# Performance work log

Hardware: AMD Instinct MI355X
Metric: run time of the kernel (lower is better)

The kernel has to match this reference:

```python
import math
import jax, jax.numpy as jnp
import numpy as np

D_MODEL = 2048
EXPAND = 2
D_INNER = EXPAND * D_MODEL          # 4096
HEADDIM = 64
NHEADS = D_INNER // HEADDIM          # 64
D_STATE = 128
CHUNK = 64
D_CONV = 4
NGROUPS = 1
X_PROJ_DIM = D_INNER + NHEADS + 2 * NGROUPS * D_STATE  # 4416
BATCH, SEQLEN = 2, 4096


def segsum(x):
    """Stable segment sum. x: (..., T) -> (..., T, T), lower-triangular, -inf above."""
    T = x.shape[-1]
    cs = jnp.cumsum(x, axis=-1)
    ss = cs[..., :, None] - cs[..., None, :]
    mask = jnp.tril(jnp.ones((T, T), dtype=bool))
    return jnp.where(mask, ss, -jnp.inf)


def ssd(X, A, B, C, block_len):
    """Chunked SSD scan (Mamba2). X:(b,l,gh,p) A:(b,l,gh) B,C:(b,l,g,n). fp32 math."""
    b, l = X.shape[0], X.shape[1]
    g = B.shape[2]
    h = X.shape[2] // g
    c = l // block_len
    X = X.astype(jnp.float32).reshape(b, c, block_len, g, h, HEADDIM)      # b c l g h p
    B = B.astype(jnp.float32).reshape(b, c, block_len, g, D_STATE)          # b c l g n
    C = C.astype(jnp.float32).reshape(b, c, block_len, g, D_STATE)
    A = A.astype(jnp.float32).reshape(b, c, block_len, g, h)
    A = jnp.transpose(A, (0, 3, 4, 1, 2))                                   # b g h c l
    A_cumsum = jnp.cumsum(A, axis=-1)
    L = jnp.exp(segsum(A))                                                  # b g h c l s
    # intra-chunk (diagonal) output
    Y_diag = jnp.einsum('bclgn,bcsgn,bghcls,bcsghp->bclghp', C, B, L, X)
    # per-chunk state contributions
    decay_states = jnp.exp(A_cumsum[..., -1:] - A_cumsum)                   # b g h c l
    states = jnp.einsum('bclgn,bghcl,bclghp->bcghpn', B, decay_states, X)
    init = jnp.zeros_like(states[:, :1])
    states = jnp.concatenate([init, states], axis=1)                         # b (c+1) g h p n
    chunk_A = jnp.pad(A_cumsum[..., -1], ((0, 0), (0, 0), (0, 0), (1, 0)))   # b g h (c+1)
    decay_chunk = jnp.exp(segsum(chunk_A))                                   # b g h (c+1) (c+1)
    new_states = jnp.einsum('bghzc,bcghpn->bzghpn', decay_chunk, states)
    states, final_state = new_states[:, :-1], new_states[:, -1]
    state_decay_out = jnp.exp(A_cumsum)                                      # b g h c l
    Y_off = jnp.einsum('bclgn,bcghpn,bghcl->bclghp', C, states, state_decay_out)
    Y = (Y_diag + Y_off).reshape(b, l, g * h, HEADDIM)
    final_state = final_state.reshape(b, g * h, HEADDIM, D_STATE)
    return Y, final_state


def setup_inputs() -> dict:
    key = jax.random.key(0)
    ks = jax.random.split(key, 8)
    s = 0.02
    u = jax.random.uniform(ks[6], (NHEADS,))
    dt0 = jnp.exp(u * (math.log(0.1) - math.log(0.001)) + math.log(0.001))
    inv_dt = dt0 + jnp.log(-jnp.expm1(-dt0))
    dt_std = NHEADS ** (-0.5)
    return {
        'x': jax.random.normal(ks[0], (BATCH, SEQLEN, D_MODEL), jnp.float32),
        'in_proj_w': jax.random.normal(ks[1], (2 * D_INNER, D_MODEL), jnp.float32) * s,
        'conv_w': jax.random.normal(ks[2], (D_INNER, D_CONV), jnp.float32) * s,
        'conv_b': jnp.zeros((D_INNER,), jnp.float32),
        'x_proj_w': jax.random.normal(ks[3], (X_PROJ_DIM, D_INNER), jnp.float32) * s,
        'dt_proj_w': jax.random.uniform(ks[4], (NHEADS, NHEADS), jnp.float32, -dt_std, dt_std),
        'dt_proj_b': inv_dt,
        'A_log': jnp.log(jnp.arange(1, NHEADS + 1, dtype=jnp.float32)),
        'D': jnp.ones((NHEADS,), jnp.float32),
        'out_proj_w': jax.random.normal(ks[5], (D_MODEL, D_INNER), jnp.float32) * s,
    }


def reference(x, in_proj_w, conv_w, conv_b, x_proj_w, dt_proj_w, dt_proj_b, A_log, D, out_proj_w):
    b, l, _ = x.shape
    xz = x @ in_proj_w.T                                   # (b,l,2*d_inner)
    x_branch, z_branch = jnp.split(xz, 2, axis=-1)
    # causal depthwise conv1d (pad left d_conv-1, truncate to seqlen)
    xt = jnp.transpose(x_branch, (0, 2, 1))                # (b,d_inner,l)
    kern = conv_w[:, None, :]                              # (d_inner,1,k)
    y = jax.lax.conv_general_dilated(
        xt, kern, window_strides=(1,), padding=[(D_CONV - 1, 0)],
        dimension_numbers=('NCH', 'OIH', 'NCH'), feature_group_count=D_INNER)
    x_branch = jnp.transpose(y + conv_b[None, :, None], (0, 2, 1))
    x_branch = jax.nn.silu(x_branch)
    proj = x_branch @ x_proj_w.T                           # (b,l,x_proj_dim)
    X = proj[..., :D_INNER].reshape(b, l, NHEADS, HEADDIM)
    dt = proj[..., D_INNER:D_INNER + NHEADS]
    Bm = proj[..., D_INNER + NHEADS:D_INNER + NHEADS + NGROUPS * D_STATE].reshape(b, l, NGROUPS, D_STATE)
    Cm = proj[..., D_INNER + NHEADS + NGROUPS * D_STATE:].reshape(b, l, NGROUPS, D_STATE)
    dt = jax.nn.softplus(dt @ dt_proj_w.T + dt_proj_b)      # (b,l,nheads)
    A = -jnp.exp(A_log)                                     # (nheads,)
    X_scaled = X * dt[..., None]
    A_scaled = A[None, None, :] * dt
    Y, _ = ssd(X_scaled, A_scaled, Bm, Cm, CHUNK)
    Y = Y.astype(x.dtype)
    Y = Y + X * D[None, None, :, None]
    Y = Y.reshape(b, l, D_INNER)
    Y = Y * jax.nn.silu(z_branch)
    return Y @ out_proj_w.T
```

## Files before the change

kernel.cpp:

```cpp
#include <hip/hip_runtime.h>

typedef __attribute__((ext_vector_type(8))) short short8;
typedef __attribute__((ext_vector_type(4))) short s16x4;
typedef __attribute__((ext_vector_type(4))) float f32x4;
typedef __attribute__((ext_vector_type(4))) unsigned int u32x4;

typedef __attribute__((address_space(3))) unsigned int lds_u32;
typedef __attribute__((address_space(1))) unsigned int glob_u32;

__device__ __forceinline__ float bf2f(unsigned short s) {
  unsigned int v = ((unsigned int)s) << 16; float f; __builtin_memcpy(&f, &v, 4); return f;
}
__device__ __forceinline__ unsigned short f2bf(float f) {
  unsigned int u; __builtin_memcpy(&u, &f, 4);
  u += 0x7fffu + ((u >> 16) & 1u);
  return (unsigned short)(u >> 16);
}
__device__ __forceinline__ unsigned int pack2bf(float lo, float hi) {
  return (unsigned int)f2bf(lo) | ((unsigned int)f2bf(hi) << 16);
}
__device__ __forceinline__ u32x4 pack8bf(f32x4 a, f32x4 b) {
  u32x4 r;
  r[0] = pack2bf(a[0], a[1]);
  r[1] = pack2bf(a[2], a[3]);
  r[2] = pack2bf(b[0], b[1]);
  r[3] = pack2bf(b[2], b[3]);
  return r;
}
__device__ __forceinline__ void ld8bf(const unsigned short* p, float* o) {
  short8 v = *(const short8*)p;
#pragma unroll
  for (int q = 0; q < 8; ++q) o[q] = bf2f((unsigned short)v[q]);
}
__device__ __forceinline__ void gl2lds16(const unsigned short* g, unsigned short* l) {
  __builtin_amdgcn_global_load_lds((const glob_u32*)g, (lds_u32*)l, 16, 0, 0);
}

#define LSEQ   4096
#define DMODEL 2048
#define DINNER 4096
#define NHEADS 64
#define PROJ_N 4416

__global__ void f2bf_kernel(const float* __restrict__ in, unsigned short* __restrict__ out, long n8) {
  long i = (long)blockIdx.x * blockDim.x + threadIdx.x;
  if (i >= n8) return;
  f32x4 a = *(const f32x4*)(in + i * 8);
  f32x4 b = *(const f32x4*)(in + i * 8 + 4);
  *(u32x4*)(out + i * 8) = pack8bf(a, b);
}

template <bool OUT_BF16>
__global__ __launch_bounds__(256) void gemm_bb(
    const unsigned short* __restrict__ A,
    const unsigned short* __restrict__ B,
    void* __restrict__ Cp, int K, int ldc, int nmax) {
  __shared__ __attribute__((aligned(16))) unsigned short Asm[128 * 32];
  __shared__ __attribute__((aligned(16))) unsigned short Bsm[128 * 32];
  const int tid = threadIdx.x;
  const int nbx = gridDim.x;
  int flat = blockIdx.y * nbx + blockIdx.x;
  const int nwg = nbx * gridDim.y;
  if ((nwg & 7) == 0) { const int cpx = nwg >> 3; flat = (flat & 7) * cpx + (flat >> 3); }
  const int m0 = (flat / nbx) * 128;
  const int n0 = (flat % nbx) * 128;

  const int wave = tid >> 6, lane = tid & 63;
  const int wm = (wave >> 1) * 64, wn = (wave & 1) * 64;
  const int quad = lane >> 4, l16 = lane & 15;
  const int rowL = tid >> 2;
  const int kk = (tid & 3) * 8;
  const long lK = K;

  int rb0 = n0 + rowL;      if (rb0 > nmax - 1) rb0 = nmax - 1;
  int rb1 = n0 + rowL + 64; if (rb1 > nmax - 1) rb1 = nmax - 1;
  const unsigned short* pa0 = A + (long)(m0 + rowL) * lK + kk;
  const unsigned short* pa1 = pa0 + 64 * lK;
  const unsigned short* pb0 = B + (long)rb0 * lK + kk;
  const unsigned short* pb1 = B + (long)rb1 * lK + kk;

  f32x4 zero = {0.f, 0.f, 0.f, 0.f};
  f32x4 acc[4][4];
#pragma unroll
  for (int i = 0; i < 4; ++i)
#pragma unroll
    for (int j = 0; j < 4; ++j) acc[i][j] = zero;

  for (int kt = 0; kt < K; kt += 32) {
    gl2lds16(pa0 + kt, Asm + tid * 8);
    gl2lds16(pa1 + kt, Asm + tid * 8 + 2048);
    gl2lds16(pb0 + kt, Bsm + tid * 8);
    gl2lds16(pb1 + kt, Bsm + tid * 8 + 2048);
    __syncthreads();
    short8 af[4], bfv[4];
#pragma unroll
    for (int i = 0; i < 4; ++i) {
      af[i]  = *(const short8*)(Asm + (wm + i * 16 + l16) * 32 + quad * 8);
      bfv[i] = *(const short8*)(Bsm + (wn + i * 16 + l16) * 32 + quad * 8);
    }
#pragma unroll
    for (int i = 0; i < 4; ++i)
#pragma unroll
      for (int j = 0; j < 4; ++j)
        acc[i][j] = __builtin_amdgcn_mfma_f32_16x16x32_bf16(af[i], bfv[j], acc[i][j], 0, 0, 0);
    __syncthreads();
  }

#pragma unroll
  for (int i = 0; i < 4; ++i) {
    const int mbase = m0 + wm + i * 16 + quad * 4;
#pragma unroll
    for (int j = 0; j < 4; ++j) {
      const int n = n0 + wn + j * 16 + l16;
      if (n < nmax) {
#pragma unroll
        for (int r = 0; r < 4; ++r) {
          const long o = (long)(mbase + r) * ldc + n;
          if (OUT_BF16) ((unsigned short*)Cp)[o] = f2bf(acc[i][j][r]);
          else          ((float*)Cp)[o] = acc[i][j][r];
        }
      }
    }
  }
}

template <bool A_F32, bool OUT_BF16>
__global__ __launch_bounds__(256) void gemm_nt(
    const void* __restrict__ Ap,
    const float* __restrict__ B,
    void* __restrict__ Cp, int K, int ldc, int nmax) {
  __shared__ __attribute__((aligned(16))) unsigned short Asm[128 * 32];
  __shared__ __attribute__((aligned(16))) unsigned short Bsm[128 * 32];
  const int tid = threadIdx.x;
  const int m0 = blockIdx.y * 128;
  const int n0 = blockIdx.x * 128;
  const int wave = tid >> 6, lane = tid & 63;
  const int wm = (wave >> 1) * 64, wn = (wave & 1) * 64;
  const int quad = lane >> 4, l16 = lane & 15;
  const int rowL = tid >> 2;
  const int kk = (tid & 3) * 8;
  const long lK = K;

  int rb0 = n0 + rowL;      if (rb0 > nmax - 1) rb0 = nmax - 1;
  int rb1 = n0 + rowL + 64; if (rb1 > nmax - 1) rb1 = nmax - 1;

  f32x4 zero = {0.f, 0.f, 0.f, 0.f};
  f32x4 acc[4][4];
#pragma unroll
  for (int i = 0; i < 4; ++i)
#pragma unroll
    for (int j = 0; j < 4; ++j) acc[i][j] = zero;

  for (int kt = 0; kt < K; kt += 32) {
    const float* pb0 = B + (long)rb0 * lK + kt + kk;
    const float* pb1 = B + (long)rb1 * lK + kt + kk;
    f32x4 b00 = *(const f32x4*)pb0;
    f32x4 b01 = *(const f32x4*)(pb0 + 4);
    f32x4 b10 = *(const f32x4*)pb1;
    f32x4 b11 = *(const f32x4*)(pb1 + 4);
    u32x4 bw0 = pack8bf(b00, b01);
    u32x4 bw1 = pack8bf(b10, b11);
    u32x4 aw0, aw1;
    if (A_F32) {
      const float* pa = (const float*)Ap + (long)(m0 + rowL) * lK + kt + kk;
      f32x4 a00 = *(const f32x4*)pa;
      f32x4 a01 = *(const f32x4*)(pa + 4);
      f32x4 a10 = *(const f32x4*)(pa + 64 * lK);
      f32x4 a11 = *(const f32x4*)(pa + 64 * lK + 4);
      aw0 = pack8bf(a00, a01);
      aw1 = pack8bf(a10, a11);
    } else {
      const unsigned short* pa = (const unsigned short*)Ap + (long)(m0 + rowL) * lK + kt + kk;
      aw0 = *(const u32x4*)pa;
      aw1 = *(const u32x4*)(pa + 64 * lK);
    }
    *(u32x4*)(Asm + tid * 8) = aw0;
    *(u32x4*)(Asm + tid * 8 + 2048) = aw1;
    *(u32x4*)(Bsm + tid * 8) = bw0;
    *(u32x4*)(Bsm + tid * 8 + 2048) = bw1;
    __syncthreads();
    short8 af[4], bfv[4];
#pragma unroll
    for (int i = 0; i < 4; ++i) {
      af[i]  = *(const short8*)(Asm + (wm + i * 16 + l16) * 32 + quad * 8);
      bfv[i] = *(const short8*)(Bsm + (wn + i * 16 + l16) * 32 + quad * 8);
    }
#pragma unroll
    for (int i = 0; i < 4; ++i)
#pragma unroll
      for (int j = 0; j < 4; ++j)
        acc[i][j] = __builtin_amdgcn_mfma_f32_16x16x32_bf16(af[i], bfv[j], acc[i][j], 0, 0, 0);
    __syncthreads();
  }

#pragma unroll
  for (int i = 0; i < 4; ++i) {
    const int mbase = m0 + wm + i * 16 + quad * 4;
#pragma unroll
    for (int j = 0; j < 4; ++j) {
      const int n = n0 + wn + j * 16 + l16;
      if (n < nmax) {
#pragma unroll
        for (int r = 0; r < 4; ++r) {
          const long o = (long)(mbase + r) * ldc + n;
          if (OUT_BF16) ((unsigned short*)Cp)[o] = f2bf(acc[i][j][r]);
          else          ((float*)Cp)[o] = acc[i][j][r];
        }
      }
    }
  }
}

__global__ void conv_silu_kernel(const unsigned short* __restrict__ xin,
                                 const float* __restrict__ cw,
                                 const float* __restrict__ cb,
                                 unsigned short* __restrict__ xout, long nv) {
  long idx = (long)blockIdx.x * blockDim.x + threadIdx.x;
  if (idx >= nv) return;
  int c8 = (int)(idx & 511);
  long row = idx >> 9;
  int l = (int)(row & (LSEQ - 1));
  int ch0 = c8 * 8;
  float acc[8];
#pragma unroll
  for (int q = 0; q < 8; ++q) acc[q] = cb[ch0 + q];
#pragma unroll
  for (int t = 0; t < 4; ++t) {
    int ll = l - 3 + t;
    if (ll >= 0) {
      float f[8];
      ld8bf(xin + (row - 3 + t) * 4096 + ch0, f);
#pragma unroll
      for (int q = 0; q < 8; ++q) acc[q] += f[q] * cw[(ch0 + q) * 4 + t];
    }
  }
  short8 o;
#pragma unroll
  for (int q = 0; q < 8; ++q) {
    float a = acc[q] / (1.f + expf(-acc[q]));
    o[q] = (short)f2bf(a);
  }
  *(short8*)(xout + row * 4096 + ch0) = o;
}

__global__ void dt_kernel(const unsigned short* __restrict__ proj,
                          const float* __restrict__ dtw,
                          const float* __restrict__ dtb,
                          float* __restrict__ dt, long n) {
  long idx = (long)blockIdx.x * blockDim.x + threadIdx.x;
  if (idx >= n) return;
  int h = (int)(idx & 63);
  long row = idx >> 6;
  const unsigned short* p = proj + row * PROJ_N + DINNER;
  float s = dtb[h];
#pragma unroll
  for (int k8 = 0; k8 < 8; ++k8) {
    float f[8];
    ld8bf(p + k8 * 8, f);
    const float* wv = dtw + h * 64 + k8 * 8;
#pragma unroll
    for (int q = 0; q < 8; ++q) s += f[q] * wv[q];
  }
  dt[idx] = (s > 20.f) ? s : log1pf(expf(s));
}


__global__ __launch_bounds__(256) void ssd_states_kernel(
    const unsigned short* __restrict__ proj,
    const float* __restrict__ dtbuf,
    const float* __restrict__ A_log,
    float* __restrict__ states,
    float* __restrict__ chdec) {
  __shared__ float Bs[64][132];
  __shared__ float Xw[64][68];
  __shared__ float csh[64];
  __shared__ float dth[64];
  const int tid = threadIdx.x;
  const int gc = blockIdx.x;
  const int h  = blockIdx.y;
  const long rowbase = (long)gc * 64;

  const float negA = -expf(A_log[h]);
  if (tid < 64) {
    float d = dtbuf[(rowbase + tid) * 64 + h];
    float v = negA * d;
#pragma unroll
    for (int off = 1; off < 64; off <<= 1) {
      float t = __shfl_up(v, off);
      if (tid >= off) v += t;
    }
    csh[tid] = v;
    dth[tid] = d;
  }
  __syncthreads();
  const float cs63 = csh[63];

  for (int idx = tid; idx < 64 * 16; idx += 256) {
    int r = idx >> 4, c8 = idx & 15;
    float f[8];
    ld8bf(proj + (rowbase + r) * PROJ_N + 4160 + c8 * 8, f);
#pragma unroll
    for (int q = 0; q < 8; ++q) Bs[r][c8 * 8 + q] = f[q];
  }
  for (int idx = tid; idx < 64 * 8; idx += 256) {
    int r = idx >> 3, c8 = idx & 7;
    float f[8];
    ld8bf(proj + (rowbase + r) * PROJ_N + h * 64 + c8 * 8, f);
    float w = dth[r] * expf(cs63 - csh[r]);
#pragma unroll
    for (int q = 0; q < 8; ++q) Xw[r][c8 * 8 + q] = w * f[q];
  }
  __syncthreads();

  const int p0 = (tid >> 4) * 4;
  const int n0 = (tid & 15) * 4;
  float a0[4][4] = {};
  float a1[4][4] = {};
  for (int j = 0; j < 64; ++j) {
    f32x4 xv = *(const f32x4*)&Xw[j][p0];
    f32x4 b0 = *(const f32x4*)&Bs[j][n0];
    f32x4 b1 = *(const f32x4*)&Bs[j][n0 + 64];
#pragma unroll
    for (int pp = 0; pp < 4; ++pp)
#pragma unroll
      for (int q = 0; q < 4; ++q) {
        a0[pp][q] += xv[pp] * b0[q];
        a1[pp][q] += xv[pp] * b1[q];
      }
  }
  float* sb = states + ((long)gc * 64 + h) * 8192;
#pragma unroll
  for (int q = 0; q < 4; ++q) {
    f32x4 t0, t1;
#pragma unroll
    for (int pp = 0; pp < 4; ++pp) { t0[pp] = a0[pp][q]; t1[pp] = a1[pp][q]; }
    *(f32x4*)(sb + (n0 + q) * 64 + p0) = t0;
    *(f32x4*)(sb + (n0 + 64 + q) * 64 + p0) = t1;
  }
  if (tid == 0) chdec[gc * 64 + h] = expf(cs63);
}

__global__ __launch_bounds__(256) void ssd_scan_kernel(
    float* __restrict__ states, const float* __restrict__ chdec) {
  const int by = blockIdx.y;
  const int b = by >> 6, h = by & 63;
  const int pn = blockIdx.x * 256 + threadIdx.x;
  float P = 0.f;
  long base = ((long)b * 64 * 64 + h) * 8192 + pn;
  for (int c = 0; c < 64; ++c) {
    long o = base + (long)c * (64 * 8192);
    float S = states[o];
    states[o] = P;
    P = chdec[(b * 64 + c) * 64 + h] * P + S;
  }
}

__global__ __launch_bounds__(512, 4) void ssd_ydo_gate_kernel(
    const unsigned short* __restrict__ proj,
    const float* __restrict__ dtbuf,
    const float* __restrict__ A_log,
    const float* __restrict__ Dv,
    const float* __restrict__ states,
    unsigned short* __restrict__ zio) {
  __shared__ __attribute__((aligned(16))) char smem[76800];
  float (*Cs)[68]          = (float(*)[68])(smem);
  float (*Scm)[68]         = (float(*)[68])(smem + 17408);
  unsigned short (*Xb)[72] = (unsigned short(*)[72])(smem + 34816);
  float* Pt                = (float*)(smem + 44032);
  float (*BsU)[68]         = (float(*)[68])(smem + 44032);

  const int tid = threadIdx.x;
  const int lane = tid & 63;
  const int gc = blockIdx.x;
  const int hbase = blockIdx.y * 16;
  const long rowbase = (long)gc * 64;

#pragma unroll
  for (int k = 0; k < 2; ++k) {
    int idx = tid + k * 512;
    int r = idx >> 4, c8 = idx & 15;
    const unsigned short* rp = proj + (rowbase + r) * PROJ_N;
    float fB[8], fC[8];
    ld8bf(rp + 4160 + c8 * 8, fB);
    ld8bf(rp + 4288 + c8 * 8, fC);
    f32x4 b0, b1, c0, c1;
#pragma unroll
    for (int q = 0; q < 4; ++q) { b0[q] = fB[q]; b1[q] = fB[q + 4]; c0[q] = fC[q]; c1[q] = fC[q + 4]; }
    *(f32x4*)&BsU[r][c8 * 8] = b0;
    *(f32x4*)&BsU[r][c8 * 8 + 4] = b1;
    *(f32x4*)&Cs[r][c8 * 8] = c0;
    *(f32x4*)&Cs[r][c8 * 8 + 4] = c1;
  }
  __syncthreads();

  const int iS = tid >> 3, t7 = tid & 7;
  float dm[8] = {};
  for (int n8 = 0; n8 < 16; ++n8) {
    f32x4 cv0 = *(const f32x4*)&Cs[iS][n8 * 8];
    f32x4 cv1 = *(const f32x4*)&Cs[iS][n8 * 8 + 4];
#pragma unroll
    for (int q = 0; q < 8; ++q) {
      int j = t7 + q * 8;
      f32x4 bv0 = *(const f32x4*)&BsU[j][n8 * 8];
      f32x4 bv1 = *(const f32x4*)&BsU[j][n8 * 8 + 4];
      dm[q] += cv0[0] * bv0[0] + cv0[1] * bv0[1] + cv0[2] * bv0[2] + cv0[3] * bv0[3]
             + cv1[0] * bv1[0] + cv1[1] * bv1[1] + cv1[2] * bv1[2] + cv1[3] * bv1[3];
    }
  }
  __syncthreads();

  const int i0 = (tid >> 4) * 2;
  const int p0 = (tid & 15) * 4;

  for (int hh = 0; hh < 16; ++hh) {
    const int h = hbase + hh;
    const float Dh = Dv[h];
    const float negA = -expf(A_log[h]);

    const float* sb2 = states + ((long)gc * 64 + h) * 8192;
    f32x4 s0 = *(const f32x4*)(sb2 + tid * 4);
    f32x4 s1 = *(const f32x4*)(sb2 + 2048 + tid * 4);
    f32x4 s2 = *(const f32x4*)(sb2 + 4096 + tid * 4);
    f32x4 s3 = *(const f32x4*)(sb2 + 6144 + tid * 4);
    short8 x8 = *(const short8*)(proj + (rowbase + iS) * PROJ_N + h * 64 + t7 * 8);
    float d = dtbuf[(rowbase + lane) * 64 + h];

    float v = negA * d;
    {
      float t;
      t = __shfl_up(v, 1);  if (lane >= 1)  v += t;
      t = __shfl_up(v, 2);  if (lane >= 2)  v += t;
      t = __shfl_up(v, 4);  if (lane >= 4)  v += t;
      t = __shfl_up(v, 8);  if (lane >= 8)  v += t;
      t = __shfl_up(v, 16); if (lane >= 16) v += t;
      t = __shfl_up(v, 32); if (lane >= 32) v += t;
    }

    *(f32x4*)&Pt[tid * 4]        = s0;
    *(f32x4*)&Pt[2048 + tid * 4] = s1;
    *(f32x4*)&Pt[4096 + tid * 4] = s2;
    *(f32x4*)&Pt[6144 + tid * 4] = s3;
    *(short8*)&Xb[iS][t7 * 8] = x8;
    {
      const float ci = __shfl(v, iS);
#pragma unroll
      for (int q = 0; q < 8; ++q) {
        int j = t7 + q * 8;
        float cj = __shfl(v, j);
        float dj = __shfl(d, j);
        Scm[iS][j] = (j <= iS) ? dm[q] * expf(ci - cj) * dj : 0.f;
      }
    }
    __syncthreads();

    const long r0w = rowbase + i0, r1w = r0w + 1;
    const long zo0 = r0w * 4096 + h * 64 + p0;
    const long zo1 = r1w * 4096 + h * 64 + p0;
    s16x4 zv0 = *(const s16x4*)&zio[zo0];
    s16x4 zv1 = *(const s16x4*)&zio[zo1];
    s16x4 xv0 = *(const s16x4*)(proj + r0w * PROJ_N + h * 64 + p0);
    s16x4 xv1 = *(const s16x4*)(proj + r1w * PROJ_N + h * 64 + p0);

    float ya0[4] = {}, ya1[4] = {};
#pragma unroll 4
    for (int j = 0; j < 64; ++j) {
      float sc0 = Scm[i0][j], sc1 = Scm[i0 + 1][j];
      s16x4 xj = *(const s16x4*)&Xb[j][p0];
#pragma unroll
      for (int k = 0; k < 4; ++k) {
        float xv = bf2f((unsigned short)xj[k]);
        ya0[k] += sc0 * xv;
        ya1[k] += sc1 * xv;
      }
    }
    float yb0[4] = {}, yb1[4] = {};
#pragma unroll 2
    for (int n8 = 0; n8 < 16; ++n8) {
      f32x4 ca0 = *(const f32x4*)&Cs[i0][n8 * 8];
      f32x4 ca1 = *(const f32x4*)&Cs[i0][n8 * 8 + 4];
      f32x4 cb0 = *(const f32x4*)&Cs[i0 + 1][n8 * 8];
      f32x4 cb1 = *(const f32x4*)&Cs[i0 + 1][n8 * 8 + 4];
#pragma unroll
      for (int q = 0; q < 8; ++q) {
        f32x4 pv = *(const f32x4*)&Pt[(n8 * 8 + q) * 64 + p0];
        float c0 = (q < 4) ? ca0[q] : ca1[q - 4];
        float c1 = (q < 4) ? cb0[q] : cb1[q - 4];
#pragma unroll
        for (int k = 0; k < 4; ++k) {
          yb0[k] += c0 * pv[k];
          yb1[k] += c1 * pv[k];
        }
      }
    }
    const float e0 = expf(__shfl(v, i0));
    const float e1 = expf(__shfl(v, i0 + 1));
    s16x4 o0, o1;
#pragma unroll
    for (int k = 0; k < 4; ++k) {
      float y = ya0[k] + e0 * yb0[k];
      float xraw = bf2f((unsigned short)xv0[k]);
      float zz = bf2f((unsigned short)zv0[k]);
      float sz = zz / (1.f + expf(-zz));
      o0[k] = (short)f2bf((y + xraw * Dh) * sz);
      y = ya1[k] + e1 * yb1[k];
      xraw = bf2f((unsigned short)xv1[k]);
      zz = bf2f((unsigned short)zv1[k]);
      sz = zz / (1.f + expf(-zz));
      o1[k] = (short)f2bf((y + xraw * Dh) * sz);
    }
    *(s16x4*)&zio[zo0] = o0;
    *(s16x4*)&zio[zo1] = o1;
    __syncthreads();
  }
}

__global__ __launch_bounds__(512) void ssd_gate_kernel(
    const unsigned short* __restrict__ proj,
    const float* __restrict__ dtbuf,
    const float* __restrict__ A_log,
    const float* __restrict__ Dv,
    unsigned short* __restrict__ zio) {
  __shared__ float st[64][128];
  __shared__ float Bs[64][128];
  __shared__ float Cs[64][128];
  __shared__ float Xs[64][64];
  __shared__ float Sc[64][64];
  __shared__ float cs[64];
  __shared__ float dtc[64];

  const int tid = threadIdx.x;
  const int bl = blockIdx.x >> 6;
  const int h = blockIdx.x & 63;
  const float negA = -expf(A_log[h]);
  const float Dh = Dv[h];

  for (int i = tid; i < 64 * 128; i += 512) (&st[0][0])[i] = 0.f;

  for (int c = 0; c < 64; ++c) {
    const long rowbase = (long)bl * LSEQ + c * 64;
    if (tid < 64) dtc[tid] = dtbuf[(rowbase + tid) * 64 + h];
    __syncthreads();
    if (tid == 0) {
      float run = 0.f;
      for (int j = 0; j < 64; ++j) { run += negA * dtc[j]; cs[j] = run; }
    }
    {
      const int j = tid >> 3;
      const int c8 = tid & 7;
      const unsigned short* rp = proj + (rowbase + j) * PROJ_N;
      const float dj = dtc[j];
#pragma unroll
      for (int q = 0; q < 8; ++q)
        Xs[j][c8 * 8 + q] = bf2f(rp[h * 64 + c8 * 8 + q]) * dj;
#pragma unroll
      for (int q = 0; q < 16; ++q) {
        Bs[j][c8 * 16 + q] = bf2f(rp[4160 + c8 * 16 + q]);
        Cs[j][c8 * 16 + q] = bf2f(rp[4288 + c8 * 16 + q]);
      }
    }
    __syncthreads();
    {
      const int i0 = (tid >> 4) * 2;
      const int j0 = (tid & 15) * 4;
      float a[2][4] = {};
      for (int n = 0; n < 128; ++n) {
        float c0 = Cs[i0][n], c1 = Cs[i0 + 1][n];
        float b0 = Bs[j0][n], b1 = Bs[j0 + 1][n], b2 = Bs[j0 + 2][n], b3 = Bs[j0 + 3][n];
        a[0][0] += c0 * b0; a[0][1] += c0 * b1; a[0][2] += c0 * b2; a[0][3] += c0 * b3;
        a[1][0] += c1 * b0; a[1][1] += c1 * b1; a[1][2] += c1 * b2; a[1][3] += c1 * b3;
      }
#pragma unroll
      for (int ii = 0; ii < 2; ++ii)
#pragma unroll
        for (int jj = 0; jj < 4; ++jj) {
          int i = i0 + ii, j = j0 + jj;
          Sc[i][j] = (j <= i) ? a[ii][jj] * expf(cs[i] - cs[j]) : 0.f;
        }
    }
    __syncthreads();
    {
      const int i0 = (tid >> 4) * 2;
      const int p0 = (tid & 15) * 4;
      float a1[2][4] = {};
      for (int j = 0; j < 64; ++j) {
        float s0 = Sc[i0][j], s1 = Sc[i0 + 1][j];
        float x0 = Xs[j][p0], x1 = Xs[j][p0 + 1], x2 = Xs[j][p0 + 2], x3 = Xs[j][p0 + 3];
        a1[0][0] += s0 * x0; a1[0][1] += s0 * x1; a1[0][2] += s0 * x2; a1[0][3] += s0 * x3;
        a1[1][0] += s1 * x0; a1[1][1] += s1 * x1; a1[1][2] += s1 * x2; a1[1][3] += s1 * x3;
      }
      float a2[2][4] = {};
      for (int n = 0; n < 128; ++n) {
        float c0 = Cs[i0][n], c1 = Cs[i0 + 1][n];
        float t0 = st[p0][n], t1 = st[p0 + 1][n], t2 = st[p0 + 2][n], t3 = st[p0 + 3][n];
        a2[0][0] += c0 * t0; a2[0][1] += c0 * t1; a2[0][2] += c0 * t2; a2[0][3] += c0 * t3;
        a2[1][0] += c1 * t0; a2[1][1] += c1 * t1; a2[1][2] += c1 * t2; a2[1][3] += c1 * t3;
      }
      float e0 = expf(cs[i0]), e1 = expf(cs[i0 + 1]);
#pragma unroll
      for (int ii = 0; ii < 2; ++ii) {
        const long r = rowbase + i0 + ii;
        const long zo = r * 4096 + h * 64 + p0;
        const unsigned short* xr = proj + r * PROJ_N + h * 64 + p0;
        float e = ii ? e1 : e0;
#pragma unroll
        for (int pp = 0; pp < 4; ++pp) {
          float y = a1[ii][pp] + e * a2[ii][pp];
          float xraw = bf2f(xr[pp]);
          float zz = bf2f(zio[zo + pp]);
          float sz = zz / (1.f + expf(-zz));
          zio[zo + pp] = f2bf((y + xraw * Dh) * sz);
        }
      }
    }
    __syncthreads();
    {
      const int j = tid >> 3;
      const int p0 = (tid & 7) * 8;
      float f = expf(cs[63] - cs[j]);
#pragma unroll
      for (int q = 0; q < 8; ++q) Xs[j][p0 + q] *= f;
    }
    __syncthreads();
    {
      const float dec = expf(cs[63]);
      const int p0 = (tid >> 5) * 4;
      const int n0 = (tid & 31) * 4;
      float a[4][4] = {};
      for (int j = 0; j < 64; ++j) {
        float x0 = Xs[j][p0], x1 = Xs[j][p0 + 1], x2 = Xs[j][p0 + 2], x3 = Xs[j][p0 + 3];
        float b0 = Bs[j][n0], b1 = Bs[j][n0 + 1], b2 = Bs[j][n0 + 2], b3 = Bs[j][n0 + 3];
        a[0][0] += x0 * b0; a[0][1] += x0 * b1; a[0][2] += x0 * b2; a[0][3] += x0 * b3;
        a[1][0] += x1 * b0; a[1][1] += x1 * b1; a[1][2] += x1 * b2; a[1][3] += x1 * b3;
        a[2][0] += x2 * b0; a[2][1] += x2 * b1; a[2][2] += x2 * b2; a[2][3] += x2 * b3;
        a[3][0] += x3 * b0; a[3][1] += x3 * b1; a[3][2] += x3 * b2; a[3][3] += x3 * b3;
      }
#pragma unroll
      for (int pp = 0; pp < 4; ++pp)
#pragma unroll
        for (int nn = 0; nn < 4; ++nn)
          st[p0 + pp][n0 + nn] = dec * st[p0 + pp][n0 + nn] + a[pp][nn];
    }
    __syncthreads();
  }
}

extern "C" void kernel_launch(void* const* d_in, const int* in_sizes, int n_in,
                              void* d_out, int out_size, void* d_ws, size_t ws_size,
                              hipStream_t stream) {
  (void)in_sizes; (void)n_in; (void)out_size;
  const float* x    = (const float*)d_in[0];
  const float* w1   = (const float*)d_in[1];
  const float* cw   = (const float*)d_in[2];
  const float* cb   = (const float*)d_in[3];
  const float* w2   = (const float*)d_in[4];
  const float* dtw  = (const float*)d_in[5];
  const float* dtb  = (const float*)d_in[6];
  const float* Alog = (const float*)d_in[7];
  const float* Dv   = (const float*)d_in[8];
  const float* w3   = (const float*)d_in[9];
  float* out = (float*)d_out;

  const size_t NEED8 = 410025984ull;
  const size_t NEED4 = 205012992ull;
  int CR; bool newpath;
  if      (ws_size >= NEED8)               { CR = 8192; newpath = true;  }
  else if (ws_size >= NEED4)               { CR = 4096; newpath = true;  }
  else if (ws_size >= (size_t)8192 * 17280){ CR = 8192; newpath = false; }
  else if (ws_size >= (size_t)4096 * 17280){ CR = 4096; newpath = false; }
  else return;

  char* w = (char*)d_ws;
  const size_t S1 = (size_t)CR * 4096 * 2;
  const size_t S2 = (size_t)CR * PROJ_N * 2;
  const int nb = CR / LSEQ;
  unsigned short* xc   = (unsigned short*)(w);
  unsigned short* xp   = (unsigned short*)(w + S1);
  unsigned short* proj = (unsigned short*)(w + S1);
  unsigned short* z    = (unsigned short*)(w);
  float* dtf           = (float*)(w + S1 + S2);
  float* chdec         = (float*)(w + S1 + S2 + (size_t)CR * 256);
  float* states        = (float*)(w + S1 + S2 + (size_t)CR * 256 + (size_t)nb * 16384);

  unsigned short* xbf  = (unsigned short*)states;
  unsigned short* w1bf = xbf + (size_t)CR * 2048;
  unsigned short* w2bf = w1bf + (size_t)8192 * 2048;
  unsigned short* w3bf = (unsigned short*)states;

  for (int r0 = 0; r0 < 8192; r0 += CR) {
    const float* xr = x + (size_t)r0 * DMODEL;
    dim3 g1(DINNER / 128, CR / 128);
    dim3 g2((PROJ_N + 127) / 128, CR / 128);
    dim3 g3(DMODEL / 128, CR / 128);
    if (newpath) {
      f2bf_kernel<<<((long)CR * 2048 / 8 + 255) / 256, 256, 0, stream>>>(xr, xbf, (long)CR * 2048 / 8);
      f2bf_kernel<<<((long)8192 * 2048 / 8 + 255) / 256, 256, 0, stream>>>(w1, w1bf, (long)8192 * 2048 / 8);
      f2bf_kernel<<<((long)4416 * 4096 / 8 + 255) / 256, 256, 0, stream>>>(w2, w2bf, (long)4416 * 4096 / 8);
      gemm_bb<true><<<g1, 256, 0, stream>>>(xbf, w1bf, xp, DMODEL, DINNER, DINNER);
      conv_silu_kernel<<<((long)CR * 512) / 256, 256, 0, stream>>>(xp, cw, cb, xc, (long)CR * 512);
      gemm_bb<true><<<g2, 256, 0, stream>>>(xc, w2bf, proj, DINNER, PROJ_N, PROJ_N);
      dt_kernel<<<((long)CR * NHEADS) / 256, 256, 0, stream>>>(proj, dtw, dtb, dtf, (long)CR * NHEADS);
      gemm_bb<true><<<g1, 256, 0, stream>>>(xbf, w1bf + (size_t)DINNER * DMODEL, z, DMODEL, DINNER, DINNER);
      ssd_states_kernel<<<dim3(nb * 64, 64), 256, 0, stream>>>(proj, dtf, Alog, states, chdec);
      ssd_scan_kernel<<<dim3(32, nb * 64), 256, 0, stream>>>(states, chdec);
      ssd_ydo_gate_kernel<<<dim3(nb * 64, 4), 512, 0, stream>>>(proj, dtf, Alog, Dv, states, z);
      f2bf_kernel<<<((long)2048 * 4096 / 8 + 255) / 256, 256, 0, stream>>>(w3, w3bf, (long)2048 * 4096 / 8);
      gemm_bb<false><<<g3, 256, 0, stream>>>(z, w3bf, out + (size_t)r0 * DMODEL, DINNER, DMODEL, DMODEL);
    } else {
      gemm_nt<true, true><<<g1, 256, 0, stream>>>(xr, w1, xp, DMODEL, DINNER, DINNER);
      conv_silu_kernel<<<((long)CR * 512) / 256, 256, 0, stream>>>(xp, cw, cb, xc, (long)CR * 512);
      gemm_nt<false, true><<<g2, 256, 0, stream>>>(xc, w2, proj, DINNER, PROJ_N, PROJ_N);
      dt_kernel<<<((long)CR * NHEADS) / 256, 256, 0, stream>>>(proj, dtw, dtb, dtf, (long)CR * NHEADS);
      gemm_nt<true, true><<<g1, 256, 0, stream>>>(xr, w1 + (size_t)DINNER * DMODEL, z, DMODEL, DINNER, DINNER);
      ssd_gate_kernel<<<(CR / LSEQ) * NHEADS, 512, 0, stream>>>(proj, dtf, Alog, Dv, z);
      gemm_nt<false, false><<<g3, 256, 0, stream>>>(z, w3, out + (size_t)r0 * DMODEL, DINNER, DMODEL, DMODEL);
    }
  }
}
```

Baseline: 2.156 ms.

## Replace bf16 GEMM with 256x256-tile double-buffered swizzled-LDS pipelined kernel

Replaces the 128x128, single-buffered, K=32 bf16 GEMM with a 256x256-tile, 512-thread kernel that uses K=64 steps and double-buffered 128KB LDS. Global-to-LDS loads are interleaved with MFMA sub-phases and tracked by explicit vmcnt waits and barriers. LDS addresses are XOR-swizzled to avoid bank conflicts, and s_setprio is raised around the MFMA phases. The aim is to overlap memory traffic with compute and increase data reuse. In exchange it adds register and LDS pressure, and the manual waitcnt and barrier sequencing is fragile.

Measured after the change: 1.921 ms. 10.9% less time.

```diff
diff --git a/kernel.cpp b/kernel.cpp
--- a/kernel.cpp
+++ b/kernel.cpp
@@ -50,78 +50,143 @@
   *(u32x4*)(out + i * 8) = pack8bf(a, b);
 }
 
-template <bool OUT_BF16>
-__global__ __launch_bounds__(256) void gemm_bb(
+#define CFENCE asm volatile("" ::: "memory")
+#define BARRIER do { CFENCE; __builtin_amdgcn_s_barrier(); CFENCE; } while (0)
+#define VMW(n) asm volatile("s_waitcnt vmcnt(" #n ")" ::: "memory")
+
+template <int MODE>
+__global__ __launch_bounds__(512, 2) void gemm256(
     const unsigned short* __restrict__ A,
     const unsigned short* __restrict__ B,
     void* __restrict__ Cp, int K, int ldc, int nmax) {
-  __shared__ __attribute__((aligned(16))) unsigned short Asm[128 * 32];
-  __shared__ __attribute__((aligned(16))) unsigned short Bsm[128 * 32];
+  __shared__ __attribute__((aligned(16))) char smem[131072];
   const int tid = threadIdx.x;
   const int nbx = gridDim.x;
   int flat = blockIdx.y * nbx + blockIdx.x;
   const int nwg = nbx * gridDim.y;
   if ((nwg & 7) == 0) { const int cpx = nwg >> 3; flat = (flat & 7) * cpx + (flat >> 3); }
-  const int m0 = (flat / nbx) * 128;
-  const int n0 = (flat % nbx) * 128;
+  const int m0 = (flat / nbx) * 256;
+  const int n0 = (flat % nbx) * 256;
 
   const int wave = tid >> 6, lane = tid & 63;
-  const int wm = (wave >> 1) * 64, wn = (wave & 1) * 64;
+  const int wm = wave >> 2;
+  const int wn = wave & 3;
   const int quad = lane >> 4, l16 = lane & 15;
-  const int rowL = tid >> 2;
-  const int kk = (tid & 3) * 8;
+
+  const int r0 = tid >> 3;
+  const int kboff = ((tid & 7) ^ (r0 & 7)) * 8;
   const long lK = K;
-
-  int rb0 = n0 + rowL;      if (rb0 > nmax - 1) rb0 = nmax - 1;
-  int rb1 = n0 + rowL + 64; if (rb1 > nmax - 1) rb1 = nmax - 1;
-  const unsigned short* pa0 = A + (long)(m0 + rowL) * lK + kk;
-  const unsigned short* pa1 = pa0 + 64 * lK;
-  const unsigned short* pb0 = B + (long)rb0 * lK + kk;
-  const unsigned short* pb1 = B + (long)rb1 * lK + kk;
-
-  f32x4 zero = {0.f, 0.f, 0.f, 0.f};
-  f32x4 acc[4][4];
-#pragma unroll
-  for (int i = 0; i < 4; ++i)
-#pragma unroll
-    for (int j = 0; j < 4; ++j) acc[i][j] = zero;
-
-  for (int kt = 0; kt < K; kt += 32) {
-    gl2lds16(pa0 + kt, Asm + tid * 8);
-    gl2lds16(pa1 + kt, Asm + tid * 8 + 2048);
-    gl2lds16(pb0 + kt, Bsm + tid * 8);
-    gl2lds16(pb1 + kt, Bsm + tid * 8 + 2048);
-    __syncthreads();
-    short8 af[4], bfv[4];
-#pragma unroll
-    for (int i = 0; i < 4; ++i) {
-      af[i]  = *(const short8*)(Asm + (wm + i * 16 + l16) * 32 + quad * 8);
-      bfv[i] = *(const short8*)(Bsm + (wn + i * 16 + l16) * 32 + quad * 8);
-    }
-#pragma unroll
-    for (int i = 0; i < 4; ++i)
-#pragma unroll
-      for (int j = 0; j < 4; ++j)
-        acc[i][j] = __builtin_amdgcn_mfma_f32_16x16x32_bf16(af[i], bfv[j], acc[i][j], 0, 0, 0);
-    __syncthreads();
-  }
-
-#pragma unroll
-  for (int i = 0; i < 4; ++i) {
-    const int mbase = m0 + wm + i * 16 + quad * 4;
+  const unsigned short* pa[4];
+  const unsigned short* pb[4];
+#pragma unroll
+  for (int h2 = 0; h2 < 4; ++h2) {
+    pa[h2] = A + (long)(m0 + h2 * 64 + r0) * lK + kboff;
+    int br = n0 + h2 * 64 + r0; if (br > nmax - 1) br = nmax - 1;
+    pb[h2] = B + (long)br * lK + kboff;
+  }
+  char* ldsp = (char*)smem;
+  const int ldst = tid * 16;
+
+#define STG_A(b, h, kt) do { \
+    gl2lds16(pa[(h)*2]     + (long)(kt) * 64, (unsigned short*)(ldsp + (b)*65536 + (h)*16384 + ldst)); \
+    gl2lds16(pa[(h)*2 + 1] + (long)(kt) * 64, (unsigned short*)(ldsp + (b)*65536 + (h)*16384 + 8192 + ldst)); \
+  } while (0)
+#define STG_B(b, h, kt) do { \
+    gl2lds16(pb[(h)*2]     + (long)(kt) * 64, (unsigned short*)(ldsp + (b)*65536 + 32768 + (h)*16384 + ldst)); \
+    gl2lds16(pb[(h)*2 + 1] + (long)(kt) * 64, (unsigned short*)(ldsp + (b)*65536 + 32768 + (h)*16384 + 8192 + ldst)); \
+  } while (0)
+
+  const int xm = (l16 & 7) << 4;
+  const int cb0 = (quad * 16) ^ xm;
+  const int cb1 = cb0 ^ 64;
+  const int aoff = (wm * 128 + l16) * 128;
+  const int boff = 32768 + (wn * 64 + l16) * 128;
+
+  f32x4 acc[8][4];
+  {
+    f32x4 z4 = {0.f, 0.f, 0.f, 0.f};
+#pragma unroll
+    for (int i = 0; i < 8; ++i)
+#pragma unroll
+      for (int j = 0; j < 4; ++j) acc[i][j] = z4;
+  }
+  short8 afr[2][2], bfr[4][2];
+
+#define LDB(b) do { \
+    const char* p_ = ldsp + (b) * 65536 + boff; \
+    _Pragma("unroll") for (int nr = 0; nr < 4; ++nr) { \
+      bfr[nr][0] = *(const short8*)(p_ + nr * 2048 + cb0); \
+      bfr[nr][1] = *(const short8*)(p_ + nr * 2048 + cb1); } \
+  } while (0)
+#define LDA(b, mq) do { \
+    const char* p_ = ldsp + (b) * 65536 + aoff + (mq) * 4096; \
+    _Pragma("unroll") for (int mr = 0; mr < 2; ++mr) { \
+      afr[mr][0] = *(const short8*)(p_ + mr * 2048 + cb0); \
+      afr[mr][1] = *(const short8*)(p_ + mr * 2048 + cb1); } \
+  } while (0)
+#define MM(mq) do { \
+    __builtin_amdgcn_s_setprio(1); \
+    _Pragma("unroll") for (int ks = 0; ks < 2; ++ks) \
+    _Pragma("unroll") for (int mr = 0; mr < 2; ++mr) \
+    _Pragma("unroll") for (int nr = 0; nr < 4; ++nr) \
+      acc[(mq) * 2 + mr][nr] = __builtin_amdgcn_mfma_f32_16x16x32_bf16( \
+          afr[mr][ks], bfr[nr][ks], acc[(mq) * 2 + mr][nr], 0, 0, 0); \
+    __builtin_amdgcn_s_setprio(0); \
+  } while (0)
+
+  const int nt = K >> 6;
+
+  STG_A(0, 0, 0); STG_A(0, 1, 0);
+  STG_B(0, 0, 0); STG_B(0, 1, 0);
+  STG_B(1, 0, 1); STG_B(1, 1, 1);
+  VMW(0);
+  BARRIER;
+
+  for (int t = 0; t < nt; t += 2) {
+    const int kt1 = t + 1;
+    const int kt2 = (t + 2 < nt) ? t + 2 : nt - 1;
+    const int kt3 = (t + 3 < nt) ? t + 3 : nt - 1;
+    LDB(0); LDA(0, 0);
+    STG_A(1, 0, kt1); STG_A(1, 1, kt1);
+    BARRIER; MM(0); BARRIER;
+    LDA(0, 1); STG_B(0, 0, kt2);
+    BARRIER; MM(1); BARRIER;
+    LDA(0, 2); STG_B(0, 1, kt2);
+    BARRIER; MM(2); BARRIER;
+    LDA(0, 3);
+    BARRIER; MM(3); VMW(4); BARRIER;
+    LDB(1); LDA(1, 0);
+    STG_A(0, 0, kt2);
+    BARRIER; MM(0); BARRIER;
+    LDA(1, 1); STG_A(0, 1, kt2);
+    BARRIER; MM(1); BARRIER;
+    LDA(1, 2); STG_B(1, 0, kt3);
+    BARRIER; MM(2); BARRIER;
+    LDA(1, 3); STG_B(1, 1, kt3);
+    BARRIER; MM(3); VMW(4); BARRIER;
+  }
+
+#pragma unroll
+  for (int i = 0; i < 8; ++i) {
+    const int mbase = m0 + wm * 128 + i * 16 + quad * 4;
 #pragma unroll
     for (int j = 0; j < 4; ++j) {
-      const int n = n0 + wn + j * 16 + l16;
+      const int n = n0 + wn * 64 + j * 16 + l16;
       if (n < nmax) {
 #pragma unroll
         for (int r = 0; r < 4; ++r) {
           const long o = (long)(mbase + r) * ldc + n;
-          if (OUT_BF16) ((unsigned short*)Cp)[o] = f2bf(acc[i][j][r]);
-          else          ((float*)Cp)[o] = acc[i][j][r];
+          if (MODE == 0) ((unsigned short*)Cp)[o] = f2bf(acc[i][j][r]);
+          else           ((float*)Cp)[o] = acc[i][j][r];
         }
       }
     }
   }
+#undef STG_A
+#undef STG_B
+#undef LDB
+#undef LDA
+#undef MM
 }
 
 template <bool A_F32, bool OUT_BF16>
@@ -688,24 +753,27 @@
 
   for (int r0 = 0; r0 < 8192; r0 += CR) {
     const float* xr = x + (size_t)r0 * DMODEL;
-    dim3 g1(DINNER / 128, CR / 128);
-    dim3 g2((PROJ_N + 127) / 128, CR / 128);
-    dim3 g3(DMODEL / 128, CR / 128);
     if (newpath) {
+      dim3 G1(DINNER / 256, CR / 256);
+      dim3 G2(18, CR / 256);
+      dim3 G3(DMODEL / 256, CR / 256);
       f2bf_kernel<<<((long)CR * 2048 / 8 + 255) / 256, 256, 0, stream>>>(xr, xbf, (long)CR * 2048 / 8);
       f2bf_kernel<<<((long)8192 * 2048 / 8 + 255) / 256, 256, 0, stream>>>(w1, w1bf, (long)8192 * 2048 / 8);
       f2bf_kernel<<<((long)4416 * 4096 / 8 + 255) / 256, 256, 0, stream>>>(w2, w2bf, (long)4416 * 4096 / 8);
-      gemm_bb<true><<<g1, 256, 0, stream>>>(xbf, w1bf, xp, DMODEL, DINNER, DINNER);
+      gemm256<0><<<G1, 512, 0, stream>>>(xbf, w1bf, xp, DMODEL, DINNER, DINNER);
       conv_silu_kernel<<<((long)CR * 512) / 256, 256, 0, stream>>>(xp, cw, cb, xc, (long)CR * 512);
-      gemm_bb<true><<<g2, 256, 0, stream>>>(xc, w2bf, proj, DINNER, PROJ_N, PROJ_N);
+      gemm256<0><<<G2, 512, 0, stream>>>(xc, w2bf, proj, DINNER, PROJ_N, PROJ_N);
       dt_kernel<<<((long)CR * NHEADS) / 256, 256, 0, stream>>>(proj, dtw, dtb, dtf, (long)CR * NHEADS);
-      gemm_bb<true><<<g1, 256, 0, stream>>>(xbf, w1bf + (size_t)DINNER * DMODEL, z, DMODEL, DINNER, DINNER);
+      gemm256<0><<<G1, 512, 0, stream>>>(xbf, w1bf + (size_t)DINNER * DMODEL, z, DMODEL, DINNER, DINNER);
       ssd_states_kernel<<<dim3(nb * 64, 64), 256, 0, stream>>>(proj, dtf, Alog, states, chdec);
       ssd_scan_kernel<<<dim3(32, nb * 64), 256, 0, stream>>>(states, chdec);
       ssd_ydo_gate_kernel<<<dim3(nb * 64, 4), 512, 0, stream>>>(proj, dtf, Alog, Dv, states, z);
       f2bf_kernel<<<((long)2048 * 4096 / 8 + 255) / 256, 256, 0, stream>>>(w3, w3bf, (long)2048 * 4096 / 8);
-      gemm_bb<false><<<g3, 256, 0, stream>>>(z, w3bf, out + (size_t)r0 * DMODEL, DINNER, DMODEL, DMODEL);
+      gemm256<1><<<G3, 512, 0, stream>>>(z, w3bf, out + (size_t)r0 * DMODEL, DINNER, DMODEL, DMODEL);
     } else {
+      dim3 g1(DINNER / 128, CR / 128);
+      dim3 g2((PROJ_N + 127) / 128, CR / 128);
+      dim3 g3(DMODEL / 128, CR / 128);
       gemm_nt<true, true><<<g1, 256, 0, stream>>>(xr, w1, xp, DMODEL, DINNER, DINNER);
       conv_silu_kernel<<<((long)CR * 512) / 256, 256, 0, stream>>>(xp, cw, cb, xc, (long)CR * 512);
       gemm_nt<false, true><<<g2, 256, 0, stream>>>(xc, w2, proj, DINNER, PROJ_N, PROJ_N);
```
